# Optimization experiments

Measured on AMD Instinct MI355X. Metric: run time of the kernel, lower is better.

The kernel has to match this reference:

```python
import jax, jax.numpy as jnp
import numpy as np

N = 100000      # nodes
K = 16          # fixed degree (num_ngbrs)
E = N * K       # edges
NFEAT = 128
NHID = 64
OPFEAT = 64


def setup_inputs() -> dict:
    key = jax.random.key(0)
    ks = jax.random.split(key, 8)
    x = jax.random.normal(ks[0], (N, NFEAT), dtype=jnp.float32)
    # edges sorted by destination node, exactly K per node (required by the
    # original e.view(-1, num_ngbrs) softmax reshape)
    edge_row = jnp.repeat(jnp.arange(N, dtype=jnp.int32), K)
    edge_col = jax.random.randint(ks[1], (E,), 0, N, dtype=jnp.int32)
    stdv1 = 1.0 / np.sqrt(NHID)
    stdv2 = 1.0 / np.sqrt(OPFEAT)
    W1 = jax.random.uniform(ks[2], (NFEAT, NHID), jnp.float32, -stdv1, stdv1)
    b1 = jax.random.uniform(ks[3], (NHID,), jnp.float32, -stdv1, stdv1)
    a1 = jax.random.normal(ks[4], (2 * NHID,), jnp.float32) * 0.1
    W2 = jax.random.uniform(ks[5], (NHID, OPFEAT), jnp.float32, -stdv2, stdv2)
    b2 = jax.random.uniform(ks[6], (OPFEAT,), jnp.float32, -stdv2, stdv2)
    a2 = jax.random.normal(ks[7], (2 * OPFEAT,), jnp.float32) * 0.1
    return {"x": x, "edge_row": edge_row, "edge_col": edge_col,
            "W1": W1, "a1": a1, "b1": b1, "W2": W2, "a2": a2, "b2": b2,
            "k": K}


def _gat_layer(x, W, a, b, edge_row, edge_col, k):
    n = x.shape[0]
    h = x @ W                                        # [N, F_out]
    # edge score: concat(h[dst], h[src]) . a  -> leaky_relu
    h_edge = jnp.concatenate([h[edge_row], h[edge_col]], axis=1)  # [E, 2F]
    e = jax.nn.leaky_relu(h_edge @ a, negative_slope=0.2)         # [E]
    # per-destination softmax over the fixed K neighbors (edges row-sorted)
    att = jax.nn.softmax(e.reshape(-1, k), axis=1).reshape(-1)    # [E]
    att = jax.lax.stop_gradient(att)  # original detaches attention
    # sparse (adj * attention) @ h  ==  segment-sum of att_e * h[src_e]
    out = jax.ops.segment_sum(att[:, None] * h[edge_col], edge_row,
                              num_segments=n)
    return out + b


def reference(x, edge_row, edge_col, W1, a1, b1, W2, a2, b2, k):
    x1 = jax.nn.relu(_gat_layer(x, W1, a1, b1, edge_row, edge_col, k))
    x2 = jax.nn.relu(_gat_layer(x1, W2, a2, b2, edge_row, edge_col, k))
    return x2
```

## Files before the change

kernel.cpp:

```cpp
#include <hip/hip_runtime.h>


typedef __attribute__((ext_vector_type(8))) _Float16 f16x8;
typedef __attribute__((ext_vector_type(4))) _Float16 f16x4;
typedef __attribute__((ext_vector_type(4))) float floatx4;

__device__ inline float ubitf(unsigned u) { union { unsigned u; float f; } v; v.u = u; return v.f; }
__device__ inline unsigned fbitu(float f) { union { float f; unsigned u; } v; v.f = f; return v.u; }

template<int KD>
__global__ __launch_bounds__(256, 2) void gemm_score_f16(
    const float* __restrict__ X, const float* __restrict__ W,
    const float* __restrict__ av, _Float16* __restrict__ H,
    float* __restrict__ s1, float* __restrict__ s2, int n)
{
    constexpr int NKT = KD / 32;
    constexpr int NF = NKT * 4 * 64;
    __shared__ f16x8 Bhi[NF];
    __shared__ f16x8 Blo[NF];
    const int tid = threadIdx.x;

    for (int f = tid; f < NF; f += 256) {
        const int ln = f & 63, ntk = f >> 6;
        const int kt = ntk >> 2, nt = ntk & 3;
        const int kbase = kt * 32 + (ln >> 4) * 8;
        const int ccol = nt * 16 + (ln & 15);
        f16x8 hh, ll;
#pragma unroll
        for (int j = 0; j < 8; j++) {
            const float w = W[(kbase + j) * 64 + ccol];
            const _Float16 wh = (_Float16)w;
            hh[j] = wh;
            ll[j] = (_Float16)(w - (float)wh);
        }
        Bhi[f] = hh; Blo[f] = ll;
    }
    __syncthreads();

    const int wave = tid >> 6, lane = tid & 63;
    const int quad = lane >> 4, l15 = lane & 15;
    const int r0 = blockIdx.x * 192 + wave * 48;

    float a1c[4], a2c[4];
#pragma unroll
    for (int nt = 0; nt < 4; nt++) {
        a1c[nt] = av[nt * 16 + l15];
        a2c[nt] = av[64 + nt * 16 + l15];
    }

    float4 raw[NKT][3][2];
#pragma unroll
    for (int rb = 0; rb < 3; rb++) {
        int ra = r0 + rb * 16 + l15; if (ra > n - 1) ra = n - 1;
        const float* xp = &X[(size_t)ra * KD + quad * 8];
#pragma unroll
        for (int kt = 0; kt < NKT; kt++) {
            raw[kt][rb][0] = *(const float4*)(xp + kt * 32);
            raw[kt][rb][1] = *(const float4*)(xp + kt * 32 + 4);
        }
    }
    f16x8 A[NKT][3];
#pragma unroll
    for (int kt = 0; kt < NKT; kt++)
#pragma unroll
        for (int rb = 0; rb < 3; rb++) {
            f16x8 a;
            a[0] = (_Float16)raw[kt][rb][0].x; a[1] = (_Float16)raw[kt][rb][0].y;
            a[2] = (_Float16)raw[kt][rb][0].z; a[3] = (_Float16)raw[kt][rb][0].w;
            a[4] = (_Float16)raw[kt][rb][1].x; a[5] = (_Float16)raw[kt][rb][1].y;
            a[6] = (_Float16)raw[kt][rb][1].z; a[7] = (_Float16)raw[kt][rb][1].w;
            A[kt][rb] = a;
        }

    floatx4 acc[4][3];
#pragma unroll
    for (int nt = 0; nt < 4; nt++)
#pragma unroll
        for (int rb = 0; rb < 3; rb++) acc[nt][rb] = (floatx4){0, 0, 0, 0};

#pragma unroll
    for (int kt = 0; kt < NKT; kt++)
#pragma unroll
        for (int nt = 0; nt < 4; nt++) {
            const f16x8 bh = Bhi[(kt * 4 + nt) * 64 + lane];
            const f16x8 bl = Blo[(kt * 4 + nt) * 64 + lane];
#pragma unroll
            for (int rb = 0; rb < 3; rb++) {
                acc[nt][rb] = __builtin_amdgcn_mfma_f32_16x16x32_f16(A[kt][rb], bh, acc[nt][rb], 0, 0, 0);
                acc[nt][rb] = __builtin_amdgcn_mfma_f32_16x16x32_f16(A[kt][rb], bl, acc[nt][rb], 0, 0, 0);
            }
        }

#pragma unroll
    for (int rb = 0; rb < 3; rb++) {
        float p1[4] = {0, 0, 0, 0}, p2[4] = {0, 0, 0, 0};
#pragma unroll
        for (int nt = 0; nt < 4; nt++)
#pragma unroll
            for (int reg = 0; reg < 4; reg++) {
                const int r = r0 + rb * 16 + quad * 4 + reg;
                if (r < n) H[(size_t)r * 64 + nt * 16 + l15] = (_Float16)acc[nt][rb][reg];
                p1[reg] = fmaf(acc[nt][rb][reg], a1c[nt], p1[reg]);
                p2[reg] = fmaf(acc[nt][rb][reg], a2c[nt], p2[reg]);
            }
#pragma unroll
        for (int m = 1; m < 16; m <<= 1)
#pragma unroll
            for (int reg = 0; reg < 4; reg++) {
                p1[reg] += __shfl_xor(p1[reg], m, 64);
                p2[reg] += __shfl_xor(p2[reg], m, 64);
            }
        if (l15 == 0)
#pragma unroll
            for (int reg = 0; reg < 4; reg++) {
                const int r = r0 + rb * 16 + quad * 4 + reg;
                if (r < n) { s1[r] = p1[reg]; s2[r] = p2[reg]; }
            }
    }
}

__global__ __launch_bounds__(256, 2) void attn_gemm_fused(
    const _Float16* __restrict__ H1, const float* __restrict__ s1a,
    const float* __restrict__ s2a, const int* __restrict__ col,
    const float* __restrict__ bias1, const float* __restrict__ W2,
    const float* __restrict__ av, _Float16* __restrict__ H2,
    float* __restrict__ s1b, float* __restrict__ s2b, int n)
{
    constexpr int NKT = 2;
    constexpr int NF = NKT * 4 * 64;
    constexpr int XST = 72;
    __shared__ f16x8 Bhi[NF];
    __shared__ f16x8 Blo[NF];
    __shared__ _Float16 Xs[4][48 * XST];
    const int tid = threadIdx.x;

    for (int f = tid; f < NF; f += 256) {
        const int ln = f & 63, ntk = f >> 6;
        const int kt = ntk >> 2, nt = ntk & 3;
        const int kbase = kt * 32 + (ln >> 4) * 8;
        const int ccol = nt * 16 + (ln & 15);
        f16x8 hh, ll;
#pragma unroll
        for (int j = 0; j < 8; j++) {
            const float w = W2[(kbase + j) * 64 + ccol];
            const _Float16 wh = (_Float16)w;
            hh[j] = wh;
            ll[j] = (_Float16)(w - (float)wh);
        }
        Bhi[f] = hh; Blo[f] = ll;
    }
    __syncthreads();

    const int wave = tid >> 6, lane = tid & 63;
    const int g = (lane >> 3) & 7, j = lane & 7;
    const int r0 = blockIdx.x * 192 + wave * 48;
    _Float16* xw = Xs[wave];

    float bb[8];
    *(float4*)&bb[0] = *(const float4*)&bias1[j * 8];
    *(float4*)&bb[4] = *(const float4*)&bias1[j * 8 + 4];

    int c0v[6], c1v[6]; float s1v[6];
#pragma unroll
    for (int ch = 0; ch < 6; ch++) {
        int dc = r0 + ch * 8 + g; if (dc > n - 1) dc = n - 1;
        c0v[ch] = col[dc * 16 + j];
        c1v[ch] = col[dc * 16 + 8 + j];
        s1v[ch] = s1a[dc];
    }
    float e0v[6], e1v[6];
#pragma unroll
    for (int ch = 0; ch < 6; ch++) {
        e0v[ch] = s1v[ch] + s2a[c0v[ch]];
        e1v[ch] = s1v[ch] + s2a[c1v[ch]];
    }
    const int bb4 = (lane & 56) << 2;
#pragma unroll
    for (int ch = 0; ch < 6; ch++) {
        float e0 = e0v[ch]; e0 = (e0 > 0.0f) ? e0 : 0.2f * e0;
        float e1 = e1v[ch]; e1 = (e1 > 0.0f) ? e1 : 0.2f * e1;
        float m = fmaxf(e0, e1);
        m = fmaxf(m, __shfl_xor(m, 1, 64));
        m = fmaxf(m, __shfl_xor(m, 2, 64));
        m = fmaxf(m, __shfl_xor(m, 4, 64));
        const float p0 = __expf(e0 - m), p1 = __expf(e1 - m);
        float s = p0 + p1;
        s += __shfl_xor(s, 1, 64); s += __shfl_xor(s, 2, 64); s += __shfl_xor(s, 4, 64);
        const float inv = 1.0f / s;
        const float att0 = p0 * inv, att1 = p1 * inv;

        int srck[16]; float attk[16];
#pragma unroll
        for (int k = 0; k < 8; k++) {
            srck[k]     = __builtin_amdgcn_ds_bpermute(bb4 + 4 * k, c0v[ch]);
            srck[k + 8] = __builtin_amdgcn_ds_bpermute(bb4 + 4 * k, c1v[ch]);
            attk[k]     = ubitf((unsigned)__builtin_amdgcn_ds_bpermute(bb4 + 4 * k, (int)fbitu(att0)));
            attk[k + 8] = ubitf((unsigned)__builtin_amdgcn_ds_bpermute(bb4 + 4 * k, (int)fbitu(att1)));
        }
        f16x8 hv[16];
#pragma unroll
        for (int k = 0; k < 16; k++)
            hv[k] = *(const f16x8*)&H1[(size_t)srck[k] * 64 + j * 8];
        float acc[8] = {0, 0, 0, 0, 0, 0, 0, 0};
#pragma unroll
        for (int k = 0; k < 16; k++)
#pragma unroll
            for (int t = 0; t < 8; t++)
                acc[t] = fmaf(attk[k], (float)hv[k][t], acc[t]);
        f16x8 xv;
#pragma unroll
        for (int t = 0; t < 8; t++)
            xv[t] = (_Float16)fmaxf(acc[t] + bb[t], 0.0f);
        *(f16x8*)&xw[(ch * 8 + g) * XST + j * 8] = xv;
    }

    const int quad = lane >> 4, l15 = lane & 15;
    float a1c[4], a2c[4];
#pragma unroll
    for (int nt = 0; nt < 4; nt++) {
        a1c[nt] = av[nt * 16 + l15];
        a2c[nt] = av[64 + nt * 16 + l15];
    }
    floatx4 acc2[4][3];
#pragma unroll
    for (int nt = 0; nt < 4; nt++)
#pragma unroll
        for (int rb = 0; rb < 3; rb++) acc2[nt][rb] = (floatx4){0, 0, 0, 0};

#pragma unroll
    for (int kt = 0; kt < NKT; kt++) {
        f16x8 A[3];
#pragma unroll
        for (int rb = 0; rb < 3; rb++)
            A[rb] = *(const f16x8*)&xw[(rb * 16 + l15) * XST + kt * 32 + quad * 8];
#pragma unroll
        for (int nt = 0; nt < 4; nt++) {
            const f16x8 bh = Bhi[(kt * 4 + nt) * 64 + lane];
            const f16x8 bl = Blo[(kt * 4 + nt) * 64 + lane];
#pragma unroll
            for (int rb = 0; rb < 3; rb++) {
                acc2[nt][rb] = __builtin_amdgcn_mfma_f32_16x16x32_f16(A[rb], bh, acc2[nt][rb], 0, 0, 0);
                acc2[nt][rb] = __builtin_amdgcn_mfma_f32_16x16x32_f16(A[rb], bl, acc2[nt][rb], 0, 0, 0);
            }
        }
    }

#pragma unroll
    for (int rb = 0; rb < 3; rb++) {
        float p1[4] = {0, 0, 0, 0}, p2[4] = {0, 0, 0, 0};
#pragma unroll
        for (int nt = 0; nt < 4; nt++)
#pragma unroll
            for (int reg = 0; reg < 4; reg++) {
                const int r = r0 + rb * 16 + quad * 4 + reg;
                if (r < n) H2[(size_t)r * 64 + nt * 16 + l15] = (_Float16)acc2[nt][rb][reg];
                p1[reg] = fmaf(acc2[nt][rb][reg], a1c[nt], p1[reg]);
                p2[reg] = fmaf(acc2[nt][rb][reg], a2c[nt], p2[reg]);
            }
#pragma unroll
        for (int m = 1; m < 16; m <<= 1)
#pragma unroll
            for (int reg = 0; reg < 4; reg++) {
                p1[reg] += __shfl_xor(p1[reg], m, 64);
                p2[reg] += __shfl_xor(p2[reg], m, 64);
            }
        if (l15 == 0)
#pragma unroll
            for (int reg = 0; reg < 4; reg++) {
                const int r = r0 + rb * 16 + quad * 4 + reg;
                if (r < n) { s1b[r] = p1[reg]; s2b[r] = p2[reg]; }
            }
    }
}

__global__ __launch_bounds__(512) void attn_final(
    const _Float16* __restrict__ H, const float* __restrict__ s1,
    const float* __restrict__ s2, const int* __restrict__ col,
    const float* __restrict__ bias, float* __restrict__ out, int n)
{
    const int lane = threadIdx.x & 63;
    const int wv = threadIdx.x >> 6;
    const int g = (lane >> 3) & 7, j = lane & 7;
    const int dst = blockIdx.x * 64 + wv * 8 + g;
    const int dc = (dst > n - 1) ? (n - 1) : dst;

    const int c0 = col[dc * 16 + j];
    const int c1 = col[dc * 16 + 8 + j];
    const float s1d = s1[dc];
    float e0 = s1d + s2[c0];
    float e1 = s1d + s2[c1];
    e0 = (e0 > 0.0f) ? e0 : 0.2f * e0;
    e1 = (e1 > 0.0f) ? e1 : 0.2f * e1;
    float m = fmaxf(e0, e1);
    m = fmaxf(m, __shfl_xor(m, 1, 64));
    m = fmaxf(m, __shfl_xor(m, 2, 64));
    m = fmaxf(m, __shfl_xor(m, 4, 64));
    const float p0 = __expf(e0 - m), p1 = __expf(e1 - m);
    float s = p0 + p1;
    s += __shfl_xor(s, 1, 64); s += __shfl_xor(s, 2, 64); s += __shfl_xor(s, 4, 64);
    const float inv = 1.0f / s;
    const float att0 = p0 * inv, att1 = p1 * inv;

    const int bb4 = (lane & 56) << 2;
    int srck[16]; float attk[16];
#pragma unroll
    for (int k = 0; k < 8; k++) {
        srck[k]     = __builtin_amdgcn_ds_bpermute(bb4 + 4 * k, c0);
        srck[k + 8] = __builtin_amdgcn_ds_bpermute(bb4 + 4 * k, c1);
        attk[k]     = ubitf((unsigned)__builtin_amdgcn_ds_bpermute(bb4 + 4 * k, (int)fbitu(att0)));
        attk[k + 8] = ubitf((unsigned)__builtin_amdgcn_ds_bpermute(bb4 + 4 * k, (int)fbitu(att1)));
    }
    f16x8 hv[16];
#pragma unroll
    for (int k = 0; k < 16; k++)
        hv[k] = *(const f16x8*)&H[(size_t)srck[k] * 64 + j * 8];
    float acc[8] = {0, 0, 0, 0, 0, 0, 0, 0};
#pragma unroll
    for (int k = 0; k < 16; k++)
#pragma unroll
        for (int t = 0; t < 8; t++)
            acc[t] = fmaf(attk[k], (float)hv[k][t], acc[t]);

    if (dst < n) {
        float4 b0 = *(const float4*)&bias[j * 8];
        float4 b1v = *(const float4*)&bias[j * 8 + 4];
        float4 o0, o1;
        o0.x = fmaxf(acc[0] + b0.x, 0.0f); o0.y = fmaxf(acc[1] + b0.y, 0.0f);
        o0.z = fmaxf(acc[2] + b0.z, 0.0f); o0.w = fmaxf(acc[3] + b0.w, 0.0f);
        o1.x = fmaxf(acc[4] + b1v.x, 0.0f); o1.y = fmaxf(acc[5] + b1v.y, 0.0f);
        o1.z = fmaxf(acc[6] + b1v.z, 0.0f); o1.w = fmaxf(acc[7] + b1v.w, 0.0f);
        *(float4*)&out[(size_t)dst * 64 + j * 8] = o0;
        *(float4*)&out[(size_t)dst * 64 + j * 8 + 4] = o1;
    }
}

extern "C" void kernel_launch(void* const* d_in, const int* in_sizes, int n_in,
                              void* d_out, int out_size, void* d_ws, size_t ws_size,
                              hipStream_t stream)
{
    const float* x        = (const float*)d_in[0];
    const int*   edge_col = (const int*)  d_in[2];
    const float* W1       = (const float*)d_in[3];
    const float* a1       = (const float*)d_in[4];
    const float* b1       = (const float*)d_in[5];
    const float* W2       = (const float*)d_in[6];
    const float* a2       = (const float*)d_in[7];
    const float* b2       = (const float*)d_in[8];
    const int n = in_sizes[0] / 128;

    _Float16* h1 = (_Float16*)d_ws;
    _Float16* h2 = h1 + (size_t)n * 64;
    float* s1a = (float*)(h2 + (size_t)n * 64);
    float* s2a = s1a + n;
    float* s1b = s2a + n;
    float* s2b = s1b + n;

    const int gemm_blocks = (n + 191) / 192;
    const int fin_blocks  = (n + 63) / 64;

    gemm_score_f16<128><<<gemm_blocks, 256, 0, stream>>>(x, W1, a1, h1, s1a, s2a, n);
    attn_gemm_fused<<<gemm_blocks, 256, 0, stream>>>(h1, s1a, s2a, edge_col, b1,
                                                     W2, a2, h2, s1b, s2b, n);
    attn_final<<<fin_blocks, 512, 0, stream>>>(h2, s1b, s2b, edge_col, b2, (float*)d_out, n);
}
```

Before: 189.3 us.

## Split fused attention-GEMM into persistent kernels with software-prefetched grid-stride loops

Unfuses the layer-1 attention and layer-2 GEMM into separate kernels, so there are now four launches, with an fp16 intermediate buffer between them. Every kernel becomes persistent, using fixed grids of 512 and 782 blocks and grid-stride loops over 16-row tiles or 8-node groups. Each loop prefetches the next iteration's X rows, col indices and s1/s2 scores in registers. The goal is to hide gather and load latency and raise occupancy by dropping the large shared staging buffer. The cost is an extra launch and an extra global round-trip of the hidden activations.

```diff
diff --git a/kernel.cpp b/kernel.cpp
--- a/kernel.cpp
+++ b/kernel.cpp
@@ -2,19 +2,17 @@
 
 
 typedef __attribute__((ext_vector_type(8))) _Float16 f16x8;
-typedef __attribute__((ext_vector_type(4))) _Float16 f16x4;
 typedef __attribute__((ext_vector_type(4))) float floatx4;
 
-__device__ inline float ubitf(unsigned u) { union { unsigned u; float f; } v; v.u = u; return v.f; }
-__device__ inline unsigned fbitu(float f) { union { float f; unsigned u; } v; v.f = f; return v.u; }
-
-template<int KD>
-__global__ __launch_bounds__(256, 2) void gemm_score_f16(
+static __device__ inline float ubitf(unsigned u) { union { unsigned u; float f; } v; v.u = u; return v.f; }
+static __device__ inline unsigned fbitu(float f) { union { float f; unsigned u; } v; v.f = f; return v.u; }
+
+__global__ __launch_bounds__(256, 4) void gemm1_score(
     const float* __restrict__ X, const float* __restrict__ W,
     const float* __restrict__ av, _Float16* __restrict__ H,
-    float* __restrict__ s1, float* __restrict__ s2, int n)
+    float* __restrict__ s1, float* __restrict__ s2, int n, int nwaves)
 {
-    constexpr int NKT = KD / 32;
+    constexpr int NKT = 4;
     constexpr int NF = NKT * 4 * 64;
     __shared__ f16x8 Bhi[NF];
     __shared__ f16x8 Blo[NF];
@@ -37,9 +35,10 @@
     }
     __syncthreads();
 
-    const int wave = tid >> 6, lane = tid & 63;
-    const int quad = lane >> 4, l15 = lane & 15;
-    const int r0 = blockIdx.x * 192 + wave * 48;
+    const int wave_g = blockIdx.x * 4 + (tid >> 6);
+    const int lane = tid & 63, quad = lane >> 4, l15 = lane & 15;
+    const int ntiles = (n + 15) / 16;
+    if (wave_g >= ntiles) return;
 
     float a1c[4], a2c[4];
 #pragma unroll
@@ -48,60 +47,59 @@
         a2c[nt] = av[64 + nt * 16 + l15];
     }
 
-    float4 raw[NKT][3][2];
-#pragma unroll
-    for (int rb = 0; rb < 3; rb++) {
-        int ra = r0 + rb * 16 + l15; if (ra > n - 1) ra = n - 1;
-        const float* xp = &X[(size_t)ra * KD + quad * 8];
+    float4 nxt[2 * NKT];
+    {
+        int r = wave_g * 16 + l15; if (r > n - 1) r = n - 1;
+        const float* xp = &X[(size_t)r * 128 + quad * 8];
 #pragma unroll
         for (int kt = 0; kt < NKT; kt++) {
-            raw[kt][rb][0] = *(const float4*)(xp + kt * 32);
-            raw[kt][rb][1] = *(const float4*)(xp + kt * 32 + 4);
-        }
-    }
-    f16x8 A[NKT][3];
-#pragma unroll
-    for (int kt = 0; kt < NKT; kt++)
-#pragma unroll
-        for (int rb = 0; rb < 3; rb++) {
+            nxt[2 * kt]     = *(const float4*)(xp + kt * 32);
+            nxt[2 * kt + 1] = *(const float4*)(xp + kt * 32 + 4);
+        }
+    }
+
+    for (int t = wave_g; t < ntiles; t += nwaves) {
+        f16x8 A[NKT];
+#pragma unroll
+        for (int kt = 0; kt < NKT; kt++) {
             f16x8 a;
-            a[0] = (_Float16)raw[kt][rb][0].x; a[1] = (_Float16)raw[kt][rb][0].y;
-            a[2] = (_Float16)raw[kt][rb][0].z; a[3] = (_Float16)raw[kt][rb][0].w;
-            a[4] = (_Float16)raw[kt][rb][1].x; a[5] = (_Float16)raw[kt][rb][1].y;
-            a[6] = (_Float16)raw[kt][rb][1].z; a[7] = (_Float16)raw[kt][rb][1].w;
-            A[kt][rb] = a;
-        }
-
-    floatx4 acc[4][3];
-#pragma unroll
-    for (int nt = 0; nt < 4; nt++)
-#pragma unroll
-        for (int rb = 0; rb < 3; rb++) acc[nt][rb] = (floatx4){0, 0, 0, 0};
-
-#pragma unroll
-    for (int kt = 0; kt < NKT; kt++)
-#pragma unroll
-        for (int nt = 0; nt < 4; nt++) {
-            const f16x8 bh = Bhi[(kt * 4 + nt) * 64 + lane];
-            const f16x8 bl = Blo[(kt * 4 + nt) * 64 + lane];
-#pragma unroll
-            for (int rb = 0; rb < 3; rb++) {
-                acc[nt][rb] = __builtin_amdgcn_mfma_f32_16x16x32_f16(A[kt][rb], bh, acc[nt][rb], 0, 0, 0);
-                acc[nt][rb] = __builtin_amdgcn_mfma_f32_16x16x32_f16(A[kt][rb], bl, acc[nt][rb], 0, 0, 0);
-            }
-        }
-
-#pragma unroll
-    for (int rb = 0; rb < 3; rb++) {
+            a[0] = (_Float16)nxt[2 * kt].x;     a[1] = (_Float16)nxt[2 * kt].y;
+            a[2] = (_Float16)nxt[2 * kt].z;     a[3] = (_Float16)nxt[2 * kt].w;
+            a[4] = (_Float16)nxt[2 * kt + 1].x; a[5] = (_Float16)nxt[2 * kt + 1].y;
+            a[6] = (_Float16)nxt[2 * kt + 1].z; a[7] = (_Float16)nxt[2 * kt + 1].w;
+            A[kt] = a;
+        }
+        const int tn = t + nwaves;
+        if (tn < ntiles) {
+            int r = tn * 16 + l15; if (r > n - 1) r = n - 1;
+            const float* xp = &X[(size_t)r * 128 + quad * 8];
+#pragma unroll
+            for (int kt = 0; kt < NKT; kt++) {
+                nxt[2 * kt]     = *(const float4*)(xp + kt * 32);
+                nxt[2 * kt + 1] = *(const float4*)(xp + kt * 32 + 4);
+            }
+        }
+
+        floatx4 acc[4] = {{0,0,0,0},{0,0,0,0},{0,0,0,0},{0,0,0,0}};
+#pragma unroll
+        for (int kt = 0; kt < NKT; kt++)
+#pragma unroll
+            for (int nt = 0; nt < 4; nt++) {
+                const f16x8 bh = Bhi[(kt * 4 + nt) * 64 + lane];
+                const f16x8 bl = Blo[(kt * 4 + nt) * 64 + lane];
+                acc[nt] = __builtin_amdgcn_mfma_f32_16x16x32_f16(A[kt], bh, acc[nt], 0, 0, 0);
+                acc[nt] = __builtin_amdgcn_mfma_f32_16x16x32_f16(A[kt], bl, acc[nt], 0, 0, 0);
+            }
+
         float p1[4] = {0, 0, 0, 0}, p2[4] = {0, 0, 0, 0};
 #pragma unroll
         for (int nt = 0; nt < 4; nt++)
 #pragma unroll
             for (int reg = 0; reg < 4; reg++) {
-                const int r = r0 + rb * 16 + quad * 4 + reg;
-                if (r < n) H[(size_t)r * 64 + nt * 16 + l15] = (_Float16)acc[nt][rb][reg];
-                p1[reg] = fmaf(acc[nt][rb][reg], a1c[nt], p1[reg]);
-                p2[reg] = fmaf(acc[nt][rb][reg], a2c[nt], p2[reg]);
+                const int r = t * 16 + quad * 4 + reg;
+                if (r < n) H[(size_t)r * 64 + nt * 16 + l15] = (_Float16)acc[nt][reg];
+                p1[reg] = fmaf(acc[nt][reg], a1c[nt], p1[reg]);
+                p2[reg] = fmaf(acc[nt][reg], a2c[nt], p2[reg]);
             }
 #pragma unroll
         for (int m = 1; m < 16; m <<= 1)
@@ -113,25 +111,21 @@
         if (l15 == 0)
 #pragma unroll
             for (int reg = 0; reg < 4; reg++) {
-                const int r = r0 + rb * 16 + quad * 4 + reg;
+                const int r = t * 16 + quad * 4 + reg;
                 if (r < n) { s1[r] = p1[reg]; s2[r] = p2[reg]; }
             }
     }
 }
 
-__global__ __launch_bounds__(256, 2) void attn_gemm_fused(
-    const _Float16* __restrict__ H1, const float* __restrict__ s1a,
-    const float* __restrict__ s2a, const int* __restrict__ col,
-    const float* __restrict__ bias1, const float* __restrict__ W2,
-    const float* __restrict__ av, _Float16* __restrict__ H2,
-    float* __restrict__ s1b, float* __restrict__ s2b, int n)
+__global__ __launch_bounds__(256, 4) void gemm2_score(
+    const _Float16* __restrict__ Xm, const float* __restrict__ W,
+    const float* __restrict__ av, _Float16* __restrict__ H,
+    float* __restrict__ s1, float* __restrict__ s2, int n, int nwaves)
 {
     constexpr int NKT = 2;
     constexpr int NF = NKT * 4 * 64;
-    constexpr int XST = 72;
     __shared__ f16x8 Bhi[NF];
     __shared__ f16x8 Blo[NF];
-    __shared__ _Float16 Xs[4][48 * XST];
     const int tid = threadIdx.x;
 
     for (int f = tid; f < NF; f += 256) {
@@ -142,7 +136,7 @@
         f16x8 hh, ll;
 #pragma unroll
         for (int j = 0; j < 8; j++) {
-            const float w = W2[(kbase + j) * 64 + ccol];
+            const float w = W[(kbase + j) * 64 + ccol];
             const _Float16 wh = (_Float16)w;
             hh[j] = wh;
             ll[j] = (_Float16)(w - (float)wh);
@@ -151,34 +145,119 @@
     }
     __syncthreads();
 
-    const int wave = tid >> 6, lane = tid & 63;
+    const int lane = tid & 63, quad = lane >> 4, l15 = lane & 15;
+    f16x8 bhr[NKT][4], blr[NKT][4];
+#pragma unroll
+    for (int kt = 0; kt < NKT; kt++)
+#pragma unroll
+        for (int nt = 0; nt < 4; nt++) {
+            bhr[kt][nt] = Bhi[(kt * 4 + nt) * 64 + lane];
+            blr[kt][nt] = Blo[(kt * 4 + nt) * 64 + lane];
+        }
+
+    const int wave_g = blockIdx.x * 4 + (tid >> 6);
+    const int ntiles = (n + 15) / 16;
+    if (wave_g >= ntiles) return;
+
+    float a1c[4], a2c[4];
+#pragma unroll
+    for (int nt = 0; nt < 4; nt++) {
+        a1c[nt] = av[nt * 16 + l15];
+        a2c[nt] = av[64 + nt * 16 + l15];
+    }
+
+    f16x8 nxt[NKT];
+    {
+        int r = wave_g * 16 + l15; if (r > n - 1) r = n - 1;
+        const _Float16* xp = &Xm[(size_t)r * 64 + quad * 8];
+#pragma unroll
+        for (int kt = 0; kt < NKT; kt++) nxt[kt] = *(const f16x8*)(xp + kt * 32);
+    }
+
+    for (int t = wave_g; t < ntiles; t += nwaves) {
+        f16x8 A[NKT];
+#pragma unroll
+        for (int kt = 0; kt < NKT; kt++) A[kt] = nxt[kt];
+        const int tn = t + nwaves;
+        if (tn < ntiles) {
+            int r = tn * 16 + l15; if (r > n - 1) r = n - 1;
+            const _Float16* xp = &Xm[(size_t)r * 64 + quad * 8];
+#pragma unroll
+            for (int kt = 0; kt < NKT; kt++) nxt[kt] = *(const f16x8*)(xp + kt * 32);
+        }
+
+        floatx4 acc[4] = {{0,0,0,0},{0,0,0,0},{0,0,0,0},{0,0,0,0}};
+#pragma unroll
+        for (int kt = 0; kt < NKT; kt++)
+#pragma unroll
+            for (int nt = 0; nt < 4; nt++) {
+                acc[nt] = __builtin_amdgcn_mfma_f32_16x16x32_f16(A[kt], bhr[kt][nt], acc[nt], 0, 0, 0);
+                acc[nt] = __builtin_amdgcn_mfma_f32_16x16x32_f16(A[kt], blr[kt][nt], acc[nt], 0, 0, 0);
+            }
+
+        float p1[4] = {0, 0, 0, 0}, p2[4] = {0, 0, 0, 0};
+#pragma unroll
+        for (int nt = 0; nt < 4; nt++)
+#pragma unroll
+            for (int reg = 0; reg < 4; reg++) {
+                const int r = t * 16 + quad * 4 + reg;
+                if (r < n) H[(size_t)r * 64 + nt * 16 + l15] = (_Float16)acc[nt][reg];
+                p1[reg] = fmaf(acc[nt][reg], a1c[nt], p1[reg]);
+                p2[reg] = fmaf(acc[nt][reg], a2c[nt], p2[reg]);
+            }
+#pragma unroll
+        for (int m = 1; m < 16; m <<= 1)
+#pragma unroll
+            for (int reg = 0; reg < 4; reg++) {
+                p1[reg] += __shfl_xor(p1[reg], m, 64);
+                p2[reg] += __shfl_xor(p2[reg], m, 64);
+            }
+        if (l15 == 0)
+#pragma unroll
+            for (int reg = 0; reg < 4; reg++) {
+                const int r = t * 16 + quad * 4 + reg;
+                if (r < n) { s1[r] = p1[reg]; s2[r] = p2[reg]; }
+            }
+    }
+}
+
+template<typename OT>
+__global__ __launch_bounds__(512, 4) void attn(
+    const _Float16* __restrict__ H, const float* __restrict__ s1,
+    const float* __restrict__ s2, const int* __restrict__ col,
+    const float* __restrict__ bias, OT* __restrict__ out, int n, int nwaves)
+{
+    const int lane = threadIdx.x & 63;
+    const int wave_g = blockIdx.x * 8 + (threadIdx.x >> 6);
     const int g = (lane >> 3) & 7, j = lane & 7;
-    const int r0 = blockIdx.x * 192 + wave * 48;
-    _Float16* xw = Xs[wave];
+    const int ngroups = (n + 7) / 8;
+    if (wave_g >= ngroups) return;
 
     float bb[8];
-    *(float4*)&bb[0] = *(const float4*)&bias1[j * 8];
-    *(float4*)&bb[4] = *(const float4*)&bias1[j * 8 + 4];
-
-    int c0v[6], c1v[6]; float s1v[6];
-#pragma unroll
-    for (int ch = 0; ch < 6; ch++) {
-        int dc = r0 + ch * 8 + g; if (dc > n - 1) dc = n - 1;
-        c0v[ch] = col[dc * 16 + j];
-        c1v[ch] = col[dc * 16 + 8 + j];
-        s1v[ch] = s1a[dc];
-    }
-    float e0v[6], e1v[6];
-#pragma unroll
-    for (int ch = 0; ch < 6; ch++) {
-        e0v[ch] = s1v[ch] + s2a[c0v[ch]];
-        e1v[ch] = s1v[ch] + s2a[c1v[ch]];
-    }
+    *(float4*)&bb[0] = *(const float4*)&bias[j * 8];
+    *(float4*)&bb[4] = *(const float4*)&bias[j * 8 + 4];
     const int bb4 = (lane & 56) << 2;
-#pragma unroll
-    for (int ch = 0; ch < 6; ch++) {
-        float e0 = e0v[ch]; e0 = (e0 > 0.0f) ? e0 : 0.2f * e0;
-        float e1 = e1v[ch]; e1 = (e1 > 0.0f) ? e1 : 0.2f * e1;
+
+    int t = wave_g;
+    int dc = t * 8 + g; if (dc > n - 1) dc = n - 1;
+    int c0 = col[dc * 16 + j];
+    int c1 = col[dc * 16 + 8 + j];
+    float s1d = s1[dc];
+    float t20 = s2[c0], t21 = s2[c1];
+
+    while (true) {
+        const int tn = t + nwaves;
+        int nc0 = 0, nc1 = 0; float ns1 = 0.0f;
+        if (tn < ngroups) {
+            int ndc = tn * 8 + g; if (ndc > n - 1) ndc = n - 1;
+            nc0 = col[ndc * 16 + j];
+            nc1 = col[ndc * 16 + 8 + j];
+            ns1 = s1[ndc];
+        }
+
+        float e0 = s1d + t20, e1 = s1d + t21;
+        e0 = (e0 > 0.0f) ? e0 : 0.2f * e0;
+        e1 = (e1 > 0.0f) ? e1 : 0.2f * e1;
         float m = fmaxf(e0, e1);
         m = fmaxf(m, __shfl_xor(m, 1, 64));
         m = fmaxf(m, __shfl_xor(m, 2, 64));
@@ -192,145 +271,47 @@
         int srck[16]; float attk[16];
 #pragma unroll
         for (int k = 0; k < 8; k++) {
-            srck[k]     = __builtin_amdgcn_ds_bpermute(bb4 + 4 * k, c0v[ch]);
-            srck[k + 8] = __builtin_amdgcn_ds_bpermute(bb4 + 4 * k, c1v[ch]);
+            srck[k]     = __builtin_amdgcn_ds_bpermute(bb4 + 4 * k, c0);
+            srck[k + 8] = __builtin_amdgcn_ds_bpermute(bb4 + 4 * k, c1);
             attk[k]     = ubitf((unsigned)__builtin_amdgcn_ds_bpermute(bb4 + 4 * k, (int)fbitu(att0)));
             attk[k + 8] = ubitf((unsigned)__builtin_amdgcn_ds_bpermute(bb4 + 4 * k, (int)fbitu(att1)));
         }
         f16x8 hv[16];
 #pragma unroll
         for (int k = 0; k < 16; k++)
-            hv[k] = *(const f16x8*)&H1[(size_t)srck[k] * 64 + j * 8];
+            hv[k] = *(const f16x8*)&H[(size_t)srck[k] * 64 + j * 8];
+
+        float nt20 = 0.0f, nt21 = 0.0f;
+        if (tn < ngroups) { nt20 = s2[nc0]; nt21 = s2[nc1]; }
+
         float acc[8] = {0, 0, 0, 0, 0, 0, 0, 0};
 #pragma unroll
         for (int k = 0; k < 16; k++)
 #pragma unroll
-            for (int t = 0; t < 8; t++)
-                acc[t] = fmaf(attk[k], (float)hv[k][t], acc[t]);
-        f16x8 xv;
-#pragma unroll
-        for (int t = 0; t < 8; t++)
-            xv[t] = (_Float16)fmaxf(acc[t] + bb[t], 0.0f);
-        *(f16x8*)&xw[(ch * 8 + g) * XST + j * 8] = xv;
-    }
-
-    const int quad = lane >> 4, l15 = lane & 15;
-    float a1c[4], a2c[4];
-#pragma unroll
-    for (int nt = 0; nt < 4; nt++) {
-        a1c[nt] = av[nt * 16 + l15];
-        a2c[nt] = av[64 + nt * 16 + l15];
-    }
-    floatx4 acc2[4][3];
-#pragma unroll
-    for (int nt = 0; nt < 4; nt++)
-#pragma unroll
-        for (int rb = 0; rb < 3; rb++) acc2[nt][rb] = (floatx4){0, 0, 0, 0};
-
-#pragma unroll
-    for (int kt = 0; kt < NKT; kt++) {
-        f16x8 A[3];
-#pragma unroll
-        for (int rb = 0; rb < 3; rb++)
-            A[rb] = *(const f16x8*)&xw[(rb * 16 + l15) * XST + kt * 32 + quad * 8];
-#pragma unroll
-        for (int nt = 0; nt < 4; nt++) {
-            const f16x8 bh = Bhi[(kt * 4 + nt) * 64 + lane];
-            const f16x8 bl = Blo[(kt * 4 + nt) * 64 + lane];
-#pragma unroll
-            for (int rb = 0; rb < 3; rb++) {
-                acc2[nt][rb] = __builtin_amdgcn_mfma_f32_16x16x32_f16(A[rb], bh, acc2[nt][rb], 0, 0, 0);
-                acc2[nt][rb] = __builtin_amdgcn_mfma_f32_16x16x32_f16(A[rb], bl, acc2[nt][rb], 0, 0, 0);
-            }
-        }
-    }
-
-#pragma unroll
-    for (int rb = 0; rb < 3; rb++) {
-        float p1[4] = {0, 0, 0, 0}, p2[4] = {0, 0, 0, 0};
-#pragma unroll
-        for (int nt = 0; nt < 4; nt++)
-#pragma unroll
-            for (int reg = 0; reg < 4; reg++) {
-                const int r = r0 + rb * 16 + quad * 4 + reg;
-                if (r < n) H2[(size_t)r * 64 + nt * 16 + l15] = (_Float16)acc2[nt][rb][reg];
-                p1[reg] = fmaf(acc2[nt][rb][reg], a1c[nt], p1[reg]);
-                p2[reg] = fmaf(acc2[nt][rb][reg], a2c[nt], p2[reg]);
-            }
-#pragma unroll
-        for (int m = 1; m < 16; m <<= 1)
-#pragma unroll
-            for (int reg = 0; reg < 4; reg++) {
-                p1[reg] += __shfl_xor(p1[reg], m, 64);
-                p2[reg] += __shfl_xor(p2[reg], m, 64);
-            }
-        if (l15 == 0)
-#pragma unroll
-            for (int reg = 0; reg < 4; reg++) {
-                const int r = r0 + rb * 16 + quad * 4 + reg;
-                if (r < n) { s1b[r] = p1[reg]; s2b[r] = p2[reg]; }
-            }
-    }
-}
-
-__global__ __launch_bounds__(512) void attn_final(
-    const _Float16* __restrict__ H, const float* __restrict__ s1,
-    const float* __restrict__ s2, const int* __restrict__ col,
-    const float* __restrict__ bias, float* __restrict__ out, int n)
-{
-    const int lane = threadIdx.x & 63;
-    const int wv = threadIdx.x >> 6;
-    const int g = (lane >> 3) & 7, j = lane & 7;
-    const int dst = blockIdx.x * 64 + wv * 8 + g;
-    const int dc = (dst > n - 1) ? (n - 1) : dst;
-
-    const int c0 = col[dc * 16 + j];
-    const int c1 = col[dc * 16 + 8 + j];
-    const float s1d = s1[dc];
-    float e0 = s1d + s2[c0];
-    float e1 = s1d + s2[c1];
-    e0 = (e0 > 0.0f) ? e0 : 0.2f * e0;
-    e1 = (e1 > 0.0f) ? e1 : 0.2f * e1;
-    float m = fmaxf(e0, e1);
-    m = fmaxf(m, __shfl_xor(m, 1, 64));
-    m = fmaxf(m, __shfl_xor(m, 2, 64));
-    m = fmaxf(m, __shfl_xor(m, 4, 64));
-    const float p0 = __expf(e0 - m), p1 = __expf(e1 - m);
-    float s = p0 + p1;
-    s += __shfl_xor(s, 1, 64); s += __shfl_xor(s, 2, 64); s += __shfl_xor(s, 4, 64);
-    const float inv = 1.0f / s;
-    const float att0 = p0 * inv, att1 = p1 * inv;
-
-    const int bb4 = (lane & 56) << 2;
-    int srck[16]; float attk[16];
-#pragma unroll
-    for (int k = 0; k < 8; k++) {
-        srck[k]     = __builtin_amdgcn_ds_bpermute(bb4 + 4 * k, c0);
-        srck[k + 8] = __builtin_amdgcn_ds_bpermute(bb4 + 4 * k, c1);
-        attk[k]     = ubitf((unsigned)__builtin_amdgcn_ds_bpermute(bb4 + 4 * k, (int)fbitu(att0)));
-        attk[k + 8] = ubitf((unsigned)__builtin_amdgcn_ds_bpermute(bb4 + 4 * k, (int)fbitu(att1)));
-    }
-    f16x8 hv[16];
-#pragma unroll
-    for (int k = 0; k < 16; k++)
-        hv[k] = *(const f16x8*)&H[(size_t)srck[k] * 64 + j * 8];
-    float acc[8] = {0, 0, 0, 0, 0, 0, 0, 0};
-#pragma unroll
-    for (int k = 0; k < 16; k++)
-#pragma unroll
-        for (int t = 0; t < 8; t++)
-            acc[t] = fmaf(attk[k], (float)hv[k][t], acc[t]);
-
-    if (dst < n) {
-        float4 b0 = *(const float4*)&bias[j * 8];
-        float4 b1v = *(const float4*)&bias[j * 8 + 4];
-        float4 o0, o1;
-        o0.x = fmaxf(acc[0] + b0.x, 0.0f); o0.y = fmaxf(acc[1] + b0.y, 0.0f);
-        o0.z = fmaxf(acc[2] + b0.z, 0.0f); o0.w = fmaxf(acc[3] + b0.w, 0.0f);
-        o1.x = fmaxf(acc[4] + b1v.x, 0.0f); o1.y = fmaxf(acc[5] + b1v.y, 0.0f);
-        o1.z = fmaxf(acc[6] + b1v.z, 0.0f); o1.w = fmaxf(acc[7] + b1v.w, 0.0f);
-        *(float4*)&out[(size_t)dst * 64 + j * 8] = o0;
-        *(float4*)&out[(size_t)dst * 64 + j * 8 + 4] = o1;
+            for (int q = 0; q < 8; q++)
+                acc[q] = fmaf(attk[k], (float)hv[k][q], acc[q]);
+
+        const int dst = t * 8 + g;
+        if (dst < n) {
+            if constexpr (sizeof(OT) == 2) {
+                f16x8 o;
+#pragma unroll
+                for (int q = 0; q < 8; q++)
+                    o[q] = (_Float16)fmaxf(acc[q] + bb[q], 0.0f);
+                *(f16x8*)&out[(size_t)dst * 64 + j * 8] = o;
+            } else {
+                float4 o0, o1;
+                o0.x = fmaxf(acc[0] + bb[0], 0.0f); o0.y = fmaxf(acc[1] + bb[1], 0.0f);
+                o0.z = fmaxf(acc[2] + bb[2], 0.0f); o0.w = fmaxf(acc[3] + bb[3], 0.0f);
+                o1.x = fmaxf(acc[4] + bb[4], 0.0f); o1.y = fmaxf(acc[5] + bb[5], 0.0f);
+                o1.z = fmaxf(acc[6] + bb[6], 0.0f); o1.w = fmaxf(acc[7] + bb[7], 0.0f);
+                *(float4*)&out[(size_t)dst * 64 + j * 8] = o0;
+                *(float4*)&out[(size_t)dst * 64 + j * 8 + 4] = o1;
+            }
+        }
+
+        if (tn >= ngroups) break;
+        t = tn; c0 = nc0; c1 = nc1; s1d = ns1; t20 = nt20; t21 = nt21;
     }
 }
 
@@ -349,17 +330,20 @@
     const int n = in_sizes[0] / 128;
 
     _Float16* h1 = (_Float16*)d_ws;
-    _Float16* h2 = h1 + (size_t)n * 64;
+    _Float16* xm = h1 + (size_t)n * 64;
+    _Float16* h2 = xm + (size_t)n * 64;
     float* s1a = (float*)(h2 + (size_t)n * 64);
     float* s2a = s1a + n;
     float* s1b = s2a + n;
     float* s2b = s1b + n;
 
-    const int gemm_blocks = (n + 191) / 192;
-    const int fin_blocks  = (n + 63) / 64;
-
-    gemm_score_f16<128><<<gemm_blocks, 256, 0, stream>>>(x, W1, a1, h1, s1a, s2a, n);
-    attn_gemm_fused<<<gemm_blocks, 256, 0, stream>>>(h1, s1a, s2a, edge_col, b1,
-                                                     W2, a2, h2, s1b, s2b, n);
-    attn_final<<<fin_blocks, 512, 0, stream>>>(h2, s1b, s2b, edge_col, b2, (float*)d_out, n);
+    const int GB = 512;
+    const int gemm_waves = GB * 4;
+    const int AB = 782;
+    const int attn_waves = AB * 8;
+
+    gemm1_score<<<GB, 256, 0, stream>>>(x, W1, a1, h1, s1a, s2a, n, gemm_waves);
+    attn<_Float16><<<AB, 512, 0, stream>>>(h1, s1a, s2a, edge_col, b1, xm, n, attn_waves);
+    gemm2_score<<<GB, 256, 0, stream>>>(xm, W2, a2, h2, s1b, s2b, n, gemm_waves);
+    attn<float><<<AB, 512, 0, stream>>>(h2, s1b, s2b, edge_col, b2, (float*)d_out, n, attn_waves);
 }
```

New measurement: 225.3 us. +19.0%, slower.
